# Optimization experiments

Measured on AMD Instinct MI355X. Metric: run time of the kernel, lower is better.

Reference implementation:

```python
import jax, jax.numpy as jnp
import numpy as np

B, S, C = 128, 4096, 64


def setup_inputs() -> dict:
    key = jax.random.key(0)
    k1, k2 = jax.random.split(key)
    logits = jax.random.normal(k1, (B, S, C), dtype=jnp.float32)
    prior_knowledge_matrix = jax.random.normal(k2, (C, C), dtype=jnp.float32)
    return {"logits": logits, "prior_knowledge_matrix": prior_knowledge_matrix}


def reference(logits, prior_knowledge_matrix):
    # log_softmax over class dim
    p = jax.nn.log_softmax(logits, axis=-1)  # [B, S, C]
    # per adjacent pair: diag(p_i @ M @ p_{i+1}^T) over the batch dim,
    # fused across all seq steps: 'bic,cd,bid->bi'
    loss_matrix = jnp.einsum("bic,cd,bid->bi", p[:, :-1, :], prior_knowledge_matrix, p[:, 1:, :])
    return loss_matrix  # [B, S-1]
```

## Files before the change

### kernel.cpp

```cpp
#include <hip/hip_runtime.h>
#include <hip/hip_bf16.h>

#define SS 4096
#define CC 64
#define PST 72
#define NROWS 129

typedef __attribute__((ext_vector_type(8))) short short8;
typedef __attribute__((ext_vector_type(4))) float floatx4;

static __device__ __forceinline__ unsigned short f2bf(float f) {
    __hip_bfloat16 h = __float2bfloat16(f);
    return *reinterpret_cast<unsigned short*>(&h);
}
static __device__ __forceinline__ float bf2f(unsigned short u) {
    __hip_bfloat16 h; *reinterpret_cast<unsigned short*>(&h) = u;
    return __bfloat162float(h);
}
static __device__ __forceinline__ float f4c(const float4& v, int k) {
    switch (k & 3) { case 0: return v.x; case 1: return v.y; case 2: return v.z; default: return v.w; }
}

#define DPP_QX1 0xB1
#define DPP_QX2 0x4E
#define DPP_HM  0x141
#define DPP_RM  0x140
template<int CTRL>
static __device__ __forceinline__ float dpp_fadd(float v) {
    int p = __builtin_amdgcn_update_dpp(0, __float_as_int(v), CTRL, 0xf, 0xf, true);
    return v + __int_as_float(p);
}
template<int CTRL>
static __device__ __forceinline__ float dpp_fmax(float v) {
    int p = __builtin_amdgcn_update_dpp(0, __float_as_int(v), CTRL, 0xf, 0xf, true);
    return fmaxf(v, __int_as_float(p));
}

__global__ __launch_bounds__(256, 4) void pkl_kernel(
        const float* __restrict__ logits,
        const float* __restrict__ M,
        float* __restrict__ out) {
    __shared__ __hip_bfloat16 mt_lds[CC * PST];
    __shared__ __hip_bfloat16 pt_lds[NROWS * PST];

    const int tid  = threadIdx.x;
    const int lane = tid & 63;
    const int w    = tid >> 6;
    const int quad = lane >> 4;
    const int nlo  = lane & 15;
    const int rq   = lane >> 2;
    const int q    = lane & 3;

    const int b  = blockIdx.x >> 5;
    const int s0 = (blockIdx.x & 31) * 128;
    const float* lg = logits + (size_t)b * SS * CC;
    const float LOG2E = 1.4426950408889634f, LN2 = 0.6931471805599453f;

    float4 xa[2][4];
    #pragma unroll
    for (int i = 0; i < 2; ++i) {
        const int lr = i * 64 + w * 16 + rq;
        const float* rp = lg + (size_t)(s0 + lr) * CC;
        #pragma unroll
        for (int j = 0; j < 4; ++j)
            xa[i][j] = *reinterpret_cast<const float4*>(rp + (j * 4 + q) * 4);
    }

    const int mc = tid >> 2;
    float mv[16];
    #pragma unroll
    for (int k = 0; k < 4; ++k)
        #pragma unroll
        for (int j = 0; j < 4; ++j)
            mv[4 * k + j] = M[mc * CC + 16 * j + 4 * q + k];
    {
        short8 g0, g1;
        #pragma unroll
        for (int o = 0; o < 8; ++o) { g0[o] = (short)f2bf(mv[o]); g1[o] = (short)f2bf(mv[o + 8]); }
        short* mp = reinterpret_cast<short*>(mt_lds) + mc * PST + 16 * q;
        *reinterpret_cast<short8*>(mp) = g0;
        *reinterpret_cast<short8*>(mp + 8) = g1;
    }

    #pragma unroll
    for (int i = 0; i < 2; ++i) {
        const int lr = i * 64 + w * 16 + rq;
        float mx = f4c(xa[i][0], 0);
        #pragma unroll
        for (int j = 0; j < 4; ++j)
            #pragma unroll
            for (int k = 0; k < 4; ++k)
                mx = fmaxf(mx, f4c(xa[i][j], k));
        mx = dpp_fmax<DPP_QX1>(mx); mx = dpp_fmax<DPP_QX2>(mx);
        float sm = 0.f;
        #pragma unroll
        for (int j = 0; j < 4; ++j)
            #pragma unroll
            for (int k = 0; k < 4; ++k)
                sm += exp2f((f4c(xa[i][j], k) - mx) * LOG2E);
        sm = dpp_fadd<DPP_QX1>(sm); sm = dpp_fadd<DPP_QX2>(sm);
        const float lse = mx + log2f(sm) * LN2;
        short8 h0, h1;
        #pragma unroll
        for (int o = 0; o < 8; ++o) {
            h0[o] = (short)f2bf(f4c(xa[i][o & 3], o >> 2) - lse);
            h1[o] = (short)f2bf(f4c(xa[i][(o + 8) & 3], (o + 8) >> 2) - lse);
        }
        short* pp = reinterpret_cast<short*>(pt_lds) + lr * PST + 16 * q;
        *reinterpret_cast<short8*>(pp) = h0;
        *reinterpret_cast<short8*>(pp + 8) = h1;
    }

    if (tid < 4) {
        const int grow = min(s0 + 128, SS - 1);
        const float* rp = lg + (size_t)grow * CC;
        float4 y[4];
        #pragma unroll
        for (int j = 0; j < 4; ++j)
            y[j] = *reinterpret_cast<const float4*>(rp + (j * 4 + tid) * 4);
        float mx = f4c(y[0], 0);
        #pragma unroll
        for (int j = 0; j < 4; ++j)
            #pragma unroll
            for (int k = 0; k < 4; ++k)
                mx = fmaxf(mx, f4c(y[j], k));
        mx = dpp_fmax<DPP_QX1>(mx); mx = dpp_fmax<DPP_QX2>(mx);
        float sm = 0.f;
        #pragma unroll
        for (int j = 0; j < 4; ++j)
            #pragma unroll
            for (int k = 0; k < 4; ++k)
                sm += exp2f((f4c(y[j], k) - mx) * LOG2E);
        sm = dpp_fadd<DPP_QX1>(sm); sm = dpp_fadd<DPP_QX2>(sm);
        const float lse = mx + log2f(sm) * LN2;
        short8 h0, h1;
        #pragma unroll
        for (int o = 0; o < 8; ++o) {
            h0[o] = (short)f2bf(f4c(y[o & 3], o >> 2) - lse);
            h1[o] = (short)f2bf(f4c(y[(o + 8) & 3], (o + 8) >> 2) - lse);
        }
        short* pp = reinterpret_cast<short*>(pt_lds) + 128 * PST + 16 * tid;
        *reinterpret_cast<short8*>(pp) = h0;
        *reinterpret_cast<short8*>(pp + 8) = h1;
    }
    __syncthreads();

    floatx4 acc[2][4];
    #pragma unroll
    for (int mt = 0; mt < 2; ++mt)
        #pragma unroll
        for (int nt = 0; nt < 4; ++nt)
            acc[mt][nt] = (floatx4){0.f, 0.f, 0.f, 0.f};

    #pragma unroll
    for (int kt = 0; kt < 2; ++kt) {
        const int koff = kt * 32 + quad * 8;
        short8 bfrag[4];
        #pragma unroll
        for (int nt = 0; nt < 4; ++nt)
            bfrag[nt] = *reinterpret_cast<const short8*>(
                reinterpret_cast<const short*>(mt_lds) + (nt * 16 + nlo) * PST + koff);
        #pragma unroll
        for (int mt = 0; mt < 2; ++mt) {
            short8 afrag = *reinterpret_cast<const short8*>(
                reinterpret_cast<const short*>(pt_lds) + (w * 32 + 1 + mt * 16 + nlo) * PST + koff);
            #pragma unroll
            for (int nt = 0; nt < 4; ++nt)
                acc[mt][nt] = __builtin_amdgcn_mfma_f32_16x16x32_bf16(
                    afrag, bfrag[nt], acc[mt][nt], 0, 0, 0);
        }
    }

    const size_t outbase = (size_t)b * (SS - 1);
    #pragma unroll
    for (int mt = 0; mt < 2; ++mt)
        #pragma unroll
        for (int r = 0; r < 4; ++r) {
            const int lrow = w * 32 + mt * 16 + quad * 4 + r;
            ushort4 pd = *reinterpret_cast<const ushort4*>(
                reinterpret_cast<const unsigned short*>(pt_lds) + lrow * PST + 4 * nlo);
            float s = bf2f(pd.x) * acc[mt][0][r] + bf2f(pd.y) * acc[mt][1][r]
                    + bf2f(pd.z) * acc[mt][2][r] + bf2f(pd.w) * acc[mt][3][r];
            s = dpp_fadd<DPP_QX1>(s); s = dpp_fadd<DPP_QX2>(s);
            s = dpp_fadd<DPP_HM>(s);  s = dpp_fadd<DPP_RM>(s);
            if (nlo == 0) {
                const int t = s0 + lrow;
                if (t <= SS - 2) out[outbase + t] = s;
            }
        }
}

extern "C" void kernel_launch(void* const* d_in, const int* in_sizes, int n_in,
                              void* d_out, int out_size, void* d_ws, size_t ws_size,
                              hipStream_t stream) {
    const float* logits = (const float*)d_in[0];
    const float* M      = (const float*)d_in[1];
    float* out          = (float*)d_out;

    dim3 grid(128 * 32), block(256);
    hipLaunchKernelGGL(pkl_kernel, grid, block, 0, stream, logits, M, out);
}
```

Baseline: 188.8 us.

## Make kernel persistent with per-wave chunks and register double-buffered prefetch

Replaces the 4096-block grid with 512 persistent blocks. Each wave independently processes 8 chunks of 32 rows using its own LDS slice, with no block-wide barriers inside the loop. The next chunk's logits are prefetched into registers while the current one is computed. The M tile is converted and loaded into MFMA B fragments once per block instead of once per 128 rows. The trade-off is higher register pressure (launch bounds lowered to 2), and the halo row is recomputed per 32-row chunk, which adds redundant softmax work.

```diff
diff --git a/kernel.cpp b/kernel.cpp
--- a/kernel.cpp
+++ b/kernel.cpp
@@ -4,7 +4,9 @@
 #define SS 4096
 #define CC 64
 #define PST 72
-#define NROWS 129
+#define WROWS 33
+#define NITER 8
+#define NBLK 512
 
 typedef __attribute__((ext_vector_type(8))) short short8;
 typedef __attribute__((ext_vector_type(4))) float floatx4;
@@ -36,12 +38,12 @@
     return fmaxf(v, __int_as_float(p));
 }
 
-__global__ __launch_bounds__(256, 4) void pkl_kernel(
+__global__ __launch_bounds__(256, 2) void pkl_kernel(
         const float* __restrict__ logits,
         const float* __restrict__ M,
         float* __restrict__ out) {
     __shared__ __hip_bfloat16 mt_lds[CC * PST];
-    __shared__ __hip_bfloat16 pt_lds[NROWS * PST];
+    __shared__ __hip_bfloat16 pt_lds[4][WROWS * PST];
 
     const int tid  = threadIdx.x;
     const int lane = tid & 63;
@@ -51,143 +53,159 @@
     const int rq   = lane >> 2;
     const int q    = lane & 3;
 
-    const int b  = blockIdx.x >> 5;
-    const int s0 = (blockIdx.x & 31) * 128;
-    const float* lg = logits + (size_t)b * SS * CC;
     const float LOG2E = 1.4426950408889634f, LN2 = 0.6931471805599453f;
 
-    float4 xa[2][4];
     #pragma unroll
-    for (int i = 0; i < 2; ++i) {
-        const int lr = i * 64 + w * 16 + rq;
-        const float* rp = lg + (size_t)(s0 + lr) * CC;
-        #pragma unroll
-        for (int j = 0; j < 4; ++j)
-            xa[i][j] = *reinterpret_cast<const float4*>(rp + (j * 4 + q) * 4);
-    }
-
-    const int mc = tid >> 2;
-    float mv[16];
-    #pragma unroll
-    for (int k = 0; k < 4; ++k)
-        #pragma unroll
-        for (int j = 0; j < 4; ++j)
-            mv[4 * k + j] = M[mc * CC + 16 * j + 4 * q + k];
-    {
-        short8 g0, g1;
-        #pragma unroll
-        for (int o = 0; o < 8; ++o) { g0[o] = (short)f2bf(mv[o]); g1[o] = (short)f2bf(mv[o + 8]); }
-        short* mp = reinterpret_cast<short*>(mt_lds) + mc * PST + 16 * q;
-        *reinterpret_cast<short8*>(mp) = g0;
-        *reinterpret_cast<short8*>(mp + 8) = g1;
-    }
-
-    #pragma unroll
-    for (int i = 0; i < 2; ++i) {
-        const int lr = i * 64 + w * 16 + rq;
-        float mx = f4c(xa[i][0], 0);
-        #pragma unroll
-        for (int j = 0; j < 4; ++j)
-            #pragma unroll
-            for (int k = 0; k < 4; ++k)
-                mx = fmaxf(mx, f4c(xa[i][j], k));
-        mx = dpp_fmax<DPP_QX1>(mx); mx = dpp_fmax<DPP_QX2>(mx);
-        float sm = 0.f;
-        #pragma unroll
-        for (int j = 0; j < 4; ++j)
-            #pragma unroll
-            for (int k = 0; k < 4; ++k)
-                sm += exp2f((f4c(xa[i][j], k) - mx) * LOG2E);
-        sm = dpp_fadd<DPP_QX1>(sm); sm = dpp_fadd<DPP_QX2>(sm);
-        const float lse = mx + log2f(sm) * LN2;
-        short8 h0, h1;
-        #pragma unroll
-        for (int o = 0; o < 8; ++o) {
-            h0[o] = (short)f2bf(f4c(xa[i][o & 3], o >> 2) - lse);
-            h1[o] = (short)f2bf(f4c(xa[i][(o + 8) & 3], (o + 8) >> 2) - lse);
-        }
-        short* pp = reinterpret_cast<short*>(pt_lds) + lr * PST + 16 * q;
-        *reinterpret_cast<short8*>(pp) = h0;
-        *reinterpret_cast<short8*>(pp + 8) = h1;
-    }
-
-    if (tid < 4) {
-        const int grow = min(s0 + 128, SS - 1);
-        const float* rp = lg + (size_t)grow * CC;
-        float4 y[4];
-        #pragma unroll
-        for (int j = 0; j < 4; ++j)
-            y[j] = *reinterpret_cast<const float4*>(rp + (j * 4 + tid) * 4);
-        float mx = f4c(y[0], 0);
-        #pragma unroll
-        for (int j = 0; j < 4; ++j)
-            #pragma unroll
-            for (int k = 0; k < 4; ++k)
-                mx = fmaxf(mx, f4c(y[j], k));
-        mx = dpp_fmax<DPP_QX1>(mx); mx = dpp_fmax<DPP_QX2>(mx);
-        float sm = 0.f;
-        #pragma unroll
-        for (int j = 0; j < 4; ++j)
-            #pragma unroll
-            for (int k = 0; k < 4; ++k)
-                sm += exp2f((f4c(y[j], k) - mx) * LOG2E);
-        sm = dpp_fadd<DPP_QX1>(sm); sm = dpp_fadd<DPP_QX2>(sm);
-        const float lse = mx + log2f(sm) * LN2;
-        short8 h0, h1;
-        #pragma unroll
-        for (int o = 0; o < 8; ++o) {
-            h0[o] = (short)f2bf(f4c(y[o & 3], o >> 2) - lse);
-            h1[o] = (short)f2bf(f4c(y[(o + 8) & 3], (o + 8) >> 2) - lse);
-        }
-        short* pp = reinterpret_cast<short*>(pt_lds) + 128 * PST + 16 * tid;
-        *reinterpret_cast<short8*>(pp) = h0;
-        *reinterpret_cast<short8*>(pp + 8) = h1;
+    for (int j = 0; j < 16; ++j) {
+        int idx = j * 256 + tid, c = idx >> 6, d = idx & 63;
+        mt_lds[c * PST + 4 * (d & 15) + (d >> 4)] = __float2bfloat16(M[idx]);
     }
     __syncthreads();
 
-    floatx4 acc[2][4];
+    short8 bfrag[2][4];
     #pragma unroll
-    for (int mt = 0; mt < 2; ++mt)
+    for (int kt = 0; kt < 2; ++kt)
         #pragma unroll
         for (int nt = 0; nt < 4; ++nt)
-            acc[mt][nt] = (floatx4){0.f, 0.f, 0.f, 0.f};
+            bfrag[kt][nt] = *reinterpret_cast<const short8*>(
+                reinterpret_cast<const short*>(mt_lds) + (nt * 16 + nlo) * PST + kt * 32 + quad * 8);
+
+    short* pw = reinterpret_cast<short*>(pt_lds[w]);
+    const int gw = blockIdx.x * 4 + w;
+
+    float4 xa[2][2][4];
+
+    {
+        const int chunk = gw;
+        const int b = chunk >> 7, s0 = (chunk & 127) * 32;
+        const float* base = logits + ((size_t)b * SS + s0) * CC;
+        #pragma unroll
+        for (int g = 0; g < 2; ++g)
+            #pragma unroll
+            for (int j = 0; j < 4; ++j)
+                xa[0][g][j] = *reinterpret_cast<const float4*>(
+                    base + (size_t)(g * 16 + rq) * CC + (j * 4 + q) * 4);
+    }
 
     #pragma unroll
-    for (int kt = 0; kt < 2; ++kt) {
-        const int koff = kt * 32 + quad * 8;
-        short8 bfrag[4];
-        #pragma unroll
-        for (int nt = 0; nt < 4; ++nt)
-            bfrag[nt] = *reinterpret_cast<const short8*>(
-                reinterpret_cast<const short*>(mt_lds) + (nt * 16 + nlo) * PST + koff);
-        #pragma unroll
-        for (int mt = 0; mt < 2; ++mt) {
-            short8 afrag = *reinterpret_cast<const short8*>(
-                reinterpret_cast<const short*>(pt_lds) + (w * 32 + 1 + mt * 16 + nlo) * PST + koff);
+    for (int it = 0; it < NITER; ++it) {
+        const int buf = it & 1;
+        const int chunk = it * 2048 + gw;
+        const int b = chunk >> 7, s0 = (chunk & 127) * 32;
+
+        if (it + 1 < NITER) {
+            const int nc = (it + 1) * 2048 + gw;
+            const int nb = nc >> 7, ns0 = (nc & 127) * 32;
+            const float* nbase = logits + ((size_t)nb * SS + ns0) * CC;
+            #pragma unroll
+            for (int g = 0; g < 2; ++g)
+                #pragma unroll
+                for (int j = 0; j < 4; ++j)
+                    xa[buf ^ 1][g][j] = *reinterpret_cast<const float4*>(
+                        nbase + (size_t)(g * 16 + rq) * CC + (j * 4 + q) * 4);
+        }
+
+        float4 xo[4];
+        const int grow = (s0 + 32 > SS - 1) ? (SS - 1) : (s0 + 32);
+        if (rq == 0) {
+            const float* op = logits + ((size_t)b * SS + grow) * CC;
+            #pragma unroll
+            for (int j = 0; j < 4; ++j)
+                xo[j] = *reinterpret_cast<const float4*>(op + (j * 4 + q) * 4);
+        }
+
+        #pragma unroll
+        for (int g = 0; g < 2; ++g) {
+            float mx = f4c(xa[buf][g][0], 0);
+            #pragma unroll
+            for (int j = 0; j < 4; ++j)
+                #pragma unroll
+                for (int k = 0; k < 4; ++k)
+                    mx = fmaxf(mx, f4c(xa[buf][g][j], k));
+            mx = dpp_fmax<DPP_QX1>(mx); mx = dpp_fmax<DPP_QX2>(mx);
+            float sm = 0.f;
+            #pragma unroll
+            for (int j = 0; j < 4; ++j)
+                #pragma unroll
+                for (int k = 0; k < 4; ++k)
+                    sm += exp2f((f4c(xa[buf][g][j], k) - mx) * LOG2E);
+            sm = dpp_fadd<DPP_QX1>(sm); sm = dpp_fadd<DPP_QX2>(sm);
+            const float lse = mx + log2f(sm) * LN2;
+            short8 h0, h1;
+            #pragma unroll
+            for (int o = 0; o < 8; ++o) {
+                h0[o] = (short)f2bf(f4c(xa[buf][g][o & 3], o >> 2) - lse);
+                h1[o] = (short)f2bf(f4c(xa[buf][g][(o + 8) & 3], (o + 8) >> 2) - lse);
+            }
+            short* pp = pw + (g * 16 + rq) * PST + 16 * q;
+            *reinterpret_cast<short8*>(pp) = h0;
+            *reinterpret_cast<short8*>(pp + 8) = h1;
+        }
+        if (rq == 0) {
+            float mx = f4c(xo[0], 0);
+            #pragma unroll
+            for (int j = 0; j < 4; ++j)
+                #pragma unroll
+                for (int k = 0; k < 4; ++k)
+                    mx = fmaxf(mx, f4c(xo[j], k));
+            mx = dpp_fmax<DPP_QX1>(mx); mx = dpp_fmax<DPP_QX2>(mx);
+            float sm = 0.f;
+            #pragma unroll
+            for (int j = 0; j < 4; ++j)
+                #pragma unroll
+                for (int k = 0; k < 4; ++k)
+                    sm += exp2f((f4c(xo[j], k) - mx) * LOG2E);
+            sm = dpp_fadd<DPP_QX1>(sm); sm = dpp_fadd<DPP_QX2>(sm);
+            const float lse = mx + log2f(sm) * LN2;
+            short8 h0, h1;
+            #pragma unroll
+            for (int o = 0; o < 8; ++o) {
+                h0[o] = (short)f2bf(f4c(xo[o & 3], o >> 2) - lse);
+                h1[o] = (short)f2bf(f4c(xo[(o + 8) & 3], (o + 8) >> 2) - lse);
+            }
+            short* pp = pw + 32 * PST + 16 * q;
+            *reinterpret_cast<short8*>(pp) = h0;
+            *reinterpret_cast<short8*>(pp + 8) = h1;
+        }
+
+        floatx4 acc[2][4];
+        #pragma unroll
+        for (int mt = 0; mt < 2; ++mt)
             #pragma unroll
             for (int nt = 0; nt < 4; ++nt)
-                acc[mt][nt] = __builtin_amdgcn_mfma_f32_16x16x32_bf16(
-                    afrag, bfrag[nt], acc[mt][nt], 0, 0, 0);
-        }
+                acc[mt][nt] = (floatx4){0.f, 0.f, 0.f, 0.f};
+        #pragma unroll
+        for (int kt = 0; kt < 2; ++kt) {
+            const int koff = kt * 32 + quad * 8;
+            #pragma unroll
+            for (int mt = 0; mt < 2; ++mt) {
+                short8 afrag = *reinterpret_cast<const short8*>(
+                    pw + (1 + mt * 16 + nlo) * PST + koff);
+                #pragma unroll
+                for (int nt = 0; nt < 4; ++nt)
+                    acc[mt][nt] = __builtin_amdgcn_mfma_f32_16x16x32_bf16(
+                        afrag, bfrag[kt][nt], acc[mt][nt], 0, 0, 0);
+            }
+        }
+
+        const size_t outbase = (size_t)b * (SS - 1);
+        #pragma unroll
+        for (int mt = 0; mt < 2; ++mt)
+            #pragma unroll
+            for (int r = 0; r < 4; ++r) {
+                const int lrow = mt * 16 + quad * 4 + r;
+                ushort4 pd = *reinterpret_cast<const ushort4*>(
+                    reinterpret_cast<const unsigned short*>(pw) + lrow * PST + 4 * nlo);
+                float s = bf2f(pd.x) * acc[mt][0][r] + bf2f(pd.y) * acc[mt][1][r]
+                        + bf2f(pd.z) * acc[mt][2][r] + bf2f(pd.w) * acc[mt][3][r];
+                s = dpp_fadd<DPP_QX1>(s); s = dpp_fadd<DPP_QX2>(s);
+                s = dpp_fadd<DPP_HM>(s);  s = dpp_fadd<DPP_RM>(s);
+                if (nlo == 0) {
+                    const int t = s0 + lrow;
+                    if (t <= SS - 2) out[outbase + t] = s;
+                }
+            }
     }
-
-    const size_t outbase = (size_t)b * (SS - 1);
-    #pragma unroll
-    for (int mt = 0; mt < 2; ++mt)
-        #pragma unroll
-        for (int r = 0; r < 4; ++r) {
-            const int lrow = w * 32 + mt * 16 + quad * 4 + r;
-            ushort4 pd = *reinterpret_cast<const ushort4*>(
-                reinterpret_cast<const unsigned short*>(pt_lds) + lrow * PST + 4 * nlo);
-            float s = bf2f(pd.x) * acc[mt][0][r] + bf2f(pd.y) * acc[mt][1][r]
-                    + bf2f(pd.z) * acc[mt][2][r] + bf2f(pd.w) * acc[mt][3][r];
-            s = dpp_fadd<DPP_QX1>(s); s = dpp_fadd<DPP_QX2>(s);
-            s = dpp_fadd<DPP_HM>(s);  s = dpp_fadd<DPP_RM>(s);
-            if (nlo == 0) {
-                const int t = s0 + lrow;
-                if (t <= SS - 2) out[outbase + t] = s;
-            }
-        }
 }
 
 extern "C" void kernel_launch(void* const* d_in, const int* in_sizes, int n_in,
@@ -197,6 +215,6 @@
     const float* M      = (const float*)d_in[1];
     float* out          = (float*)d_out;
 
-    dim3 grid(128 * 32), block(256);
+    dim3 grid(NBLK), block(256);
     hipLaunchKernelGGL(pkl_kernel, grid, block, 0, stream, logits, M, out);
 }
```

Result: slower. 194.1 us (+2.8%).
